# Kernel optimization log

Hardware: AMD Instinct MI355X
Metric: run time of the kernel (lower is better)

## Reference

```python
import jax, jax.numpy as jnp
import numpy as np

IN_F, OUT_F, GROUP = 4096, 11008, 128
N_GROUPS = IN_F // GROUP  # 32 (in_features divisible by group_size -> no padding)


def setup_inputs() -> dict:
    key = jax.random.key(0)
    kx, kw, ks, kb = jax.random.split(key, 4)
    x = jax.random.normal(kx, (4, 2048, IN_F), dtype=jnp.float32)
    weight_q = jax.random.randint(kw, (OUT_F, IN_F), -128, 128, dtype=jnp.int32).astype(jnp.int8)
    scales = jax.random.uniform(ks, (OUT_F, N_GROUPS), dtype=jnp.float32) * 0.01 + 1e-4
    bias = jax.random.normal(kb, (OUT_F,), dtype=jnp.float32)
    return {"x": x, "weight_q": weight_q, "scales": scales, "bias": bias}


def reference(x, weight_q, scales, bias):
    # Dequantize: group-wise scale along in_features, cast to fp16 (as torch .half())
    W = (weight_q.astype(jnp.float32).reshape(OUT_F, N_GROUPS, GROUP)
         * scales[:, :, None]).reshape(OUT_F, IN_F).astype(jnp.float16)
    # fp16 linear: y = x W^T + b, then back to fp32
    y = jnp.einsum('bsi,oi->bso', x.astype(jnp.float16), W) + bias.astype(jnp.float16)
    return y.astype(jnp.float32)
```

## Files before the change

### kernel.cpp

```cpp
#include <hip/hip_runtime.h>

#define IN_F 4096
#define OUT_F 11008
#define NGROUPS 32
#define M_TOTAL 8192
#define BM 256
#define BN 256
#define BK 64
#define NKT (IN_F / BK)

typedef _Float16 half_t;
typedef __attribute__((ext_vector_type(8))) _Float16 half8;
typedef __attribute__((ext_vector_type(4))) _Float16 half4v;
typedef __attribute__((ext_vector_type(4))) float f32x4;
typedef __attribute__((ext_vector_type(4))) int i32x4;

typedef __attribute__((address_space(1))) const void gvoid_t;
typedef __attribute__((address_space(3))) void lvoid_t;

__global__ void convert_x_k(const float* __restrict__ x, half_t* __restrict__ xh) {
  const int n4 = M_TOTAL * IN_F / 4;
  int stride = gridDim.x * blockDim.x;
  for (int i = blockIdx.x * blockDim.x + threadIdx.x; i < n4; i += stride) {
    f32x4 v = __builtin_nontemporal_load((const f32x4*)x + i);
    half4v h;
    h[0] = (_Float16)v[0]; h[1] = (_Float16)v[1];
    h[2] = (_Float16)v[2]; h[3] = (_Float16)v[3];
    ((half4v*)xh)[i] = h;
  }
}

__global__ void dequant_w_k(const int* __restrict__ wq,
                            const float* __restrict__ scales,
                            half_t* __restrict__ wh) {
  int row = blockIdx.x;
  int t = threadIdx.x;
  size_t base = (size_t)row * IN_F + (size_t)t * 8;
  float s = scales[row * NGROUPS + (t >> 4)];
  i32x4 q0 = __builtin_nontemporal_load((const i32x4*)(wq + base));
  i32x4 q1 = __builtin_nontemporal_load((const i32x4*)(wq + base) + 1);
  half8 h;
#pragma unroll
  for (int j = 0; j < 4; ++j) h[j] = (_Float16)((float)q0[j] * s);
#pragma unroll
  for (int j = 0; j < 4; ++j) h[4 + j] = (_Float16)((float)q1[j] * s);
  *(half8*)(wh + base) = h;
}


__device__ __forceinline__ void rd4(half8 (&d)[4], const char* base) {
#pragma unroll
  for (int i = 0; i < 4; ++i) d[i] = *(const half8*)(base + i * 1024);
}

__device__ __forceinline__ void mfma16(f32x4 (&acc)[8][4], const half8 (&a)[4],
                                       const half8 (&b)[4], int mh) {
#pragma unroll
  for (int i = 0; i < 4; ++i)
#pragma unroll
    for (int j = 0; j < 4; ++j)
      acc[mh * 4 + i][j] =
          __builtin_amdgcn_mfma_f32_16x16x32_f16(a[i], b[j], acc[mh * 4 + i][j], 0, 0, 0);
}

#define BAR() __builtin_amdgcn_s_barrier()
#define VMCNT(N) asm volatile("s_waitcnt vmcnt(" #N ")" ::: "memory")
#define PHASE_TAIL()                                   \
  do {                                                 \
    BAR();                                             \
    asm volatile("s_waitcnt lgkmcnt(0)" ::: "memory"); \
    __builtin_amdgcn_sched_barrier(0);                 \
    __builtin_amdgcn_s_setprio(1);                     \
  } while (0)
#define PHASE_END()                \
  do {                             \
    __builtin_amdgcn_s_setprio(0); \
    BAR();                         \
  } while (0)

#define STAGE(OP, KH, KT, S)                                                          \
  do {                                                                                \
    const half_t* g_ = ((OP) ? pBsrc : pAsrc) + (KT) * 64 + (KH) * 32;                \
    char* d_ = (char*)&lds[S][OP][KH][0] + wvoff;                                     \
    __builtin_amdgcn_global_load_lds((gvoid_t*)g_, (lvoid_t*)d_, 16, 0, 0);           \
    __builtin_amdgcn_global_load_lds((gvoid_t*)(g_ + 128 * IN_F),                     \
                                     (lvoid_t*)(d_ + 8192), 16, 0, 0);                \
  } while (0)

__global__ __launch_bounds__(512, 2) void gemm_k(const half_t* __restrict__ A,
                                                 const half_t* __restrict__ B,
                                                 const float* __restrict__ bias,
                                                 float* __restrict__ C) {
  __shared__ __align__(16) half_t lds[2][2][2][8192];

  const int tid = threadIdx.x;
  const int lane = tid & 63;
  const int wv = tid >> 6;
  const int wm = wv >> 2;
  const int wn = wv & 3;
  const int wvoff = wv << 10;

  const int nwg = gridDim.x;
  const int swz = ((int)(blockIdx.x & 7)) * (nwg >> 3) + ((int)blockIdx.x >> 3);
  const int bm = swz & 31;
  const int bn = swz >> 5;
  const int row0 = bm * BM;
  const int col0 = bn * BN;

  const int c16 = (tid & 3) * 16;
  const int srow = tid >> 2;
  const int clog = c16 ^ ((srow & 6) << 3);
  const int kidx = clog >> 1;
  const half_t* pAsrc = A + (size_t)(row0 + srow) * IN_F + kidx;
  const half_t* pBsrc = B + (size_t)(col0 + srow) * IN_F + kidx;

  const int r16 = lane & 15;
  const int kg = lane >> 4;
  const int arow = wm * 128 + r16;
  const int brow = wn * 64 + r16;
  const int aoff = arow * 64 + ((kg * 16) ^ ((arow & 6) << 3));
  const int boff = brow * 64 + ((kg * 16) ^ ((brow & 6) << 3));

  f32x4 acc[8][4];
#pragma unroll
  for (int m = 0; m < 8; ++m)
#pragma unroll
    for (int n = 0; n < 4; ++n) acc[m][n] = (f32x4){0.f, 0.f, 0.f, 0.f};

  STAGE(0, 0, 0, 0);
  STAGE(1, 0, 0, 0);
  STAGE(0, 1, 0, 0);
  STAGE(1, 1, 0, 0);
  STAGE(1, 0, 1, 1);
  STAGE(0, 0, 1, 1);
  STAGE(1, 1, 1, 1);
  VMCNT(6);
  BAR();

  half8 a[4], b[4];
  for (int t = 0; t < NKT - 2; ++t) {
    const int s = t & 1, ns = s ^ 1;
    const char* Ab0 = (const char*)&lds[s][0][0][0];
    const char* Bb0 = (const char*)&lds[s][1][0][0];
    const char* Ab1 = (const char*)&lds[s][0][1][0];
    const char* Bb1 = (const char*)&lds[s][1][1][0];
    rd4(a, Ab0 + aoff);
    rd4(b, Bb0 + boff);
    STAGE(0, 1, t + 1, ns);
    PHASE_TAIL();
    mfma16(acc, a, b, 0);
    PHASE_END();
    rd4(a, Ab0 + aoff + 4096);
    STAGE(1, 0, t + 2, s);
    PHASE_TAIL();
    mfma16(acc, a, b, 1);
    PHASE_END();
    rd4(a, Ab1 + aoff);
    rd4(b, Bb1 + boff);
    STAGE(0, 0, t + 2, s);
    PHASE_TAIL();
    mfma16(acc, a, b, 0);
    PHASE_END();
    rd4(a, Ab1 + aoff + 4096);
    STAGE(1, 1, t + 2, s);
    PHASE_TAIL();
    mfma16(acc, a, b, 1);
    __builtin_amdgcn_s_setprio(0);
    VMCNT(6);
    BAR();
  }

  {
    const char* Ab0 = (const char*)&lds[0][0][0][0];
    const char* Bb0 = (const char*)&lds[0][1][0][0];
    const char* Ab1 = (const char*)&lds[0][0][1][0];
    const char* Bb1 = (const char*)&lds[0][1][1][0];
    rd4(a, Ab0 + aoff);
    rd4(b, Bb0 + boff);
    STAGE(0, 1, NKT - 1, 1);
    PHASE_TAIL();
    mfma16(acc, a, b, 0);
    PHASE_END();
    rd4(a, Ab0 + aoff + 4096);
    PHASE_TAIL();
    mfma16(acc, a, b, 1);
    PHASE_END();
    rd4(a, Ab1 + aoff);
    rd4(b, Bb1 + boff);
    PHASE_TAIL();
    mfma16(acc, a, b, 0);
    PHASE_END();
    rd4(a, Ab1 + aoff + 4096);
    PHASE_TAIL();
    mfma16(acc, a, b, 1);
    __builtin_amdgcn_s_setprio(0);
    VMCNT(0);
    BAR();
  }
  {
    const char* Ab0 = (const char*)&lds[1][0][0][0];
    const char* Bb0 = (const char*)&lds[1][1][0][0];
    const char* Ab1 = (const char*)&lds[1][0][1][0];
    const char* Bb1 = (const char*)&lds[1][1][1][0];
    rd4(a, Ab0 + aoff);
    rd4(b, Bb0 + boff);
    PHASE_TAIL();
    mfma16(acc, a, b, 0);
    PHASE_END();
    rd4(a, Ab0 + aoff + 4096);
    PHASE_TAIL();
    mfma16(acc, a, b, 1);
    PHASE_END();
    rd4(a, Ab1 + aoff);
    rd4(b, Bb1 + boff);
    PHASE_TAIL();
    mfma16(acc, a, b, 0);
    PHASE_END();
    rd4(a, Ab1 + aoff + 4096);
    PHASE_TAIL();
    mfma16(acc, a, b, 1);
    PHASE_END();
  }

  const int kg4 = kg * 4;
#pragma unroll
  for (int nf = 0; nf < 4; ++nf) {
    int col = col0 + wn * 64 + nf * 16 + r16;
    _Float16 bh = (_Float16)bias[col];
#pragma unroll
    for (int mf = 0; mf < 8; ++mf) {
      int rb = row0 + wm * 128 + mf * 16 + kg4;
#pragma unroll
      for (int r = 0; r < 4; ++r) {
        _Float16 v = (_Float16)acc[mf][nf][r] + bh;
        __builtin_nontemporal_store((float)v, &C[(size_t)(rb + r) * OUT_F + col]);
      }
    }
  }
}

__global__ void naive_k(const float* __restrict__ x, const int* __restrict__ wq,
                        const float* __restrict__ scales, const float* __restrict__ bias,
                        float* __restrict__ out) {
  long idx = (long)blockIdx.x * blockDim.x + threadIdx.x;
  if (idx >= (long)M_TOTAL * OUT_F) return;
  int m = (int)(idx / OUT_F);
  int n = (int)(idx % OUT_F);
  float acc = 0.f;
  for (int g = 0; g < NGROUPS; ++g) {
    float s = scales[n * NGROUPS + g];
    for (int k = g * 128; k < (g + 1) * 128; ++k) {
      _Float16 xv = (_Float16)x[(size_t)m * IN_F + k];
      _Float16 wv = (_Float16)((float)wq[(size_t)n * IN_F + k] * s);
      acc += (float)xv * (float)wv;
    }
  }
  _Float16 r = (_Float16)acc + (_Float16)bias[n];
  out[idx] = (float)r;
}

extern "C" void kernel_launch(void* const* d_in, const int* in_sizes, int n_in,
                              void* d_out, int out_size, void* d_ws, size_t ws_size,
                              hipStream_t stream) {
  const float* x = (const float*)d_in[0];
  const int* wq = (const int*)d_in[1];
  const float* scales = (const float*)d_in[2];
  const float* bias = (const float*)d_in[3];
  float* out = (float*)d_out;

  const size_t xh_bytes = (size_t)M_TOTAL * IN_F * sizeof(half_t);
  const size_t wh_bytes = (size_t)OUT_F * IN_F * sizeof(half_t);

  if (ws_size >= xh_bytes + wh_bytes) {
    half_t* xh = (half_t*)d_ws;
    half_t* wh = (half_t*)((char*)d_ws + xh_bytes);
    convert_x_k<<<2048, 256, 0, stream>>>(x, xh);
    dequant_w_k<<<OUT_F, 512, 0, stream>>>(wq, scales, wh);
    gemm_k<<<(M_TOTAL / BM) * (OUT_F / BN), 512, 0, stream>>>(xh, wh, bias, out);
  } else {
    long total = (long)M_TOTAL * OUT_F;
    naive_k<<<(int)((total + 255) / 256), 256, 0, stream>>>(x, wq, scales, bias, out);
  }
}
```

Before: 826.9 us.

## Double-buffer LDS fragment reads in registers and use partial lgkmcnt waits

Restructures the main GEMM loop so LDS-to-register fragment reads for the next MFMA phase are issued before the current phase's MFMAs, using two register sets (aR0/aR1, bR0/bR1) and partial lgkmcnt waits instead of full waits. Each phase now has one barrier instead of two, and the global-to-LDS staging order and vmcnt accounting are re-sequenced to match. The aim is to hide LDS read latency behind matrix math and cut barrier overhead. In exchange it raises register pressure under 512-thread, 2-block launch bounds and depends on subtle wait counts for correctness.

```diff
diff --git a/kernel.cpp b/kernel.cpp
--- a/kernel.cpp
+++ b/kernel.cpp
@@ -64,19 +64,11 @@
 }
 
 #define BAR() __builtin_amdgcn_s_barrier()
+#define SB0() __builtin_amdgcn_sched_barrier(0)
+#define PRIO1() __builtin_amdgcn_s_setprio(1)
+#define PRIO0() __builtin_amdgcn_s_setprio(0)
 #define VMCNT(N) asm volatile("s_waitcnt vmcnt(" #N ")" ::: "memory")
-#define PHASE_TAIL()                                   \
-  do {                                                 \
-    BAR();                                             \
-    asm volatile("s_waitcnt lgkmcnt(0)" ::: "memory"); \
-    __builtin_amdgcn_sched_barrier(0);                 \
-    __builtin_amdgcn_s_setprio(1);                     \
-  } while (0)
-#define PHASE_END()                \
-  do {                             \
-    __builtin_amdgcn_s_setprio(0); \
-    BAR();                         \
-  } while (0)
+#define LGKM(N) asm volatile("s_waitcnt lgkmcnt(" #N ")" ::: "memory")
 
 #define STAGE(OP, KH, KT, S)                                                          \
   do {                                                                                \
@@ -131,43 +123,46 @@
   STAGE(1, 0, 0, 0);
   STAGE(0, 1, 0, 0);
   STAGE(1, 1, 0, 0);
+  STAGE(0, 0, 1, 1);
   STAGE(1, 0, 1, 1);
-  STAGE(0, 0, 1, 1);
-  STAGE(1, 1, 1, 1);
-  VMCNT(6);
+  VMCNT(8);
   BAR();
-
-  half8 a[4], b[4];
+  SB0();
+
+  half8 aR0[4], aR1[4], bR0[4], bR1[4];
+  rd4(aR0, (const char*)&lds[0][0][0][0] + aoff);
+  rd4(bR0, (const char*)&lds[0][1][0][0] + boff);
+
   for (int t = 0; t < NKT - 2; ++t) {
     const int s = t & 1, ns = s ^ 1;
     const char* Ab0 = (const char*)&lds[s][0][0][0];
     const char* Bb0 = (const char*)&lds[s][1][0][0];
     const char* Ab1 = (const char*)&lds[s][0][1][0];
     const char* Bb1 = (const char*)&lds[s][1][1][0];
-    rd4(a, Ab0 + aoff);
-    rd4(b, Bb0 + boff);
+    const char* Ab0n = (const char*)&lds[ns][0][0][0];
+    const char* Bb0n = (const char*)&lds[ns][1][0][0];
+    rd4(aR1, Ab0 + aoff + 4096);
     STAGE(0, 1, t + 1, ns);
-    PHASE_TAIL();
-    mfma16(acc, a, b, 0);
-    PHASE_END();
-    rd4(a, Ab0 + aoff + 4096);
+    LGKM(4); SB0(); PRIO1();
+    mfma16(acc, aR0, bR0, 0);
+    PRIO0(); VMCNT(6); BAR(); SB0();
+    rd4(aR0, Ab1 + aoff);
+    rd4(bR1, Bb1 + boff);
+    STAGE(1, 1, t + 1, ns);
+    LGKM(8); SB0(); PRIO1();
+    mfma16(acc, aR1, bR0, 1);
+    PRIO0(); VMCNT(6); BAR(); SB0();
+    rd4(aR1, Ab1 + aoff + 4096);
+    STAGE(0, 0, t + 2, s);
+    LGKM(4); SB0(); PRIO1();
+    mfma16(acc, aR0, bR1, 0);
+    PRIO0(); VMCNT(6); BAR(); SB0();
+    rd4(aR0, Ab0n + aoff);
+    rd4(bR0, Bb0n + boff);
     STAGE(1, 0, t + 2, s);
-    PHASE_TAIL();
-    mfma16(acc, a, b, 1);
-    PHASE_END();
-    rd4(a, Ab1 + aoff);
-    rd4(b, Bb1 + boff);
-    STAGE(0, 0, t + 2, s);
-    PHASE_TAIL();
-    mfma16(acc, a, b, 0);
-    PHASE_END();
-    rd4(a, Ab1 + aoff + 4096);
-    STAGE(1, 1, t + 2, s);
-    PHASE_TAIL();
-    mfma16(acc, a, b, 1);
-    __builtin_amdgcn_s_setprio(0);
-    VMCNT(6);
-    BAR();
+    LGKM(8); SB0(); PRIO1();
+    mfma16(acc, aR1, bR1, 1);
+    PRIO0(); VMCNT(6); BAR(); SB0();
   }
 
   {
@@ -175,51 +170,45 @@
     const char* Bb0 = (const char*)&lds[0][1][0][0];
     const char* Ab1 = (const char*)&lds[0][0][1][0];
     const char* Bb1 = (const char*)&lds[0][1][1][0];
-    rd4(a, Ab0 + aoff);
-    rd4(b, Bb0 + boff);
-    STAGE(0, 1, NKT - 1, 1);
-    PHASE_TAIL();
-    mfma16(acc, a, b, 0);
-    PHASE_END();
-    rd4(a, Ab0 + aoff + 4096);
-    PHASE_TAIL();
-    mfma16(acc, a, b, 1);
-    PHASE_END();
-    rd4(a, Ab1 + aoff);
-    rd4(b, Bb1 + boff);
-    PHASE_TAIL();
-    mfma16(acc, a, b, 0);
-    PHASE_END();
-    rd4(a, Ab1 + aoff + 4096);
-    PHASE_TAIL();
-    mfma16(acc, a, b, 1);
-    __builtin_amdgcn_s_setprio(0);
-    VMCNT(0);
-    BAR();
+    const char* Ab0n = (const char*)&lds[1][0][0][0];
+    const char* Bb0n = (const char*)&lds[1][1][0][0];
+    rd4(aR1, Ab0 + aoff + 4096);
+    STAGE(0, 1, 63, 1);
+    LGKM(4); SB0(); PRIO1();
+    mfma16(acc, aR0, bR0, 0);
+    PRIO0(); VMCNT(6); BAR(); SB0();
+    rd4(aR0, Ab1 + aoff);
+    rd4(bR1, Bb1 + boff);
+    STAGE(1, 1, 63, 1);
+    LGKM(8); SB0(); PRIO1();
+    mfma16(acc, aR1, bR0, 1);
+    PRIO0(); VMCNT(6); BAR(); SB0();
+    rd4(aR1, Ab1 + aoff + 4096);
+    LGKM(4); SB0(); PRIO1();
+    mfma16(acc, aR0, bR1, 0);
+    PRIO0(); VMCNT(4); BAR(); SB0();
+    rd4(aR0, Ab0n + aoff);
+    rd4(bR0, Bb0n + boff);
+    LGKM(8); SB0(); PRIO1();
+    mfma16(acc, aR1, bR1, 1);
+    PRIO0(); VMCNT(0); BAR(); SB0();
   }
   {
     const char* Ab0 = (const char*)&lds[1][0][0][0];
-    const char* Bb0 = (const char*)&lds[1][1][0][0];
     const char* Ab1 = (const char*)&lds[1][0][1][0];
     const char* Bb1 = (const char*)&lds[1][1][1][0];
-    rd4(a, Ab0 + aoff);
-    rd4(b, Bb0 + boff);
-    PHASE_TAIL();
-    mfma16(acc, a, b, 0);
-    PHASE_END();
-    rd4(a, Ab0 + aoff + 4096);
-    PHASE_TAIL();
-    mfma16(acc, a, b, 1);
-    PHASE_END();
-    rd4(a, Ab1 + aoff);
-    rd4(b, Bb1 + boff);
-    PHASE_TAIL();
-    mfma16(acc, a, b, 0);
-    PHASE_END();
-    rd4(a, Ab1 + aoff + 4096);
-    PHASE_TAIL();
-    mfma16(acc, a, b, 1);
-    PHASE_END();
+    rd4(aR1, Ab0 + aoff + 4096);
+    LGKM(4); SB0();
+    mfma16(acc, aR0, bR0, 0);
+    rd4(aR0, Ab1 + aoff);
+    rd4(bR1, Bb1 + boff);
+    LGKM(8); SB0();
+    mfma16(acc, aR1, bR0, 1);
+    rd4(aR1, Ab1 + aoff + 4096);
+    LGKM(4); SB0();
+    mfma16(acc, aR0, bR1, 0);
+    LGKM(0); SB0();
+    mfma16(acc, aR1, bR1, 1);
   }
 
   const int kg4 = kg * 4;
```

Measured after the change: 800.0 us. 3.3% less time.
